# Performance work log

Hardware: AMD Instinct MI355X
Metric: run time of the kernel (lower is better)

## Reference

```python
import jax, jax.numpy as jnp
import numpy as np

B, L, D, H, NE, M = 4, 1024, 768, 12, 42, 8
P = NE * (NE - 1)
OFFSET = 1  # BERT [CLS] offset, matching self.offset = 1
EPS = 1e-5


def setup_inputs() -> dict:
    key = jax.random.key(0)
    k1, k2, k3, k4 = jax.random.split(key, 4)
    sequence_output = jax.random.normal(k1, (B, L, D), dtype=jnp.float32)
    # post-softmax attention probs are nonnegative
    attention = jax.random.uniform(k2, (B, H, L, L), dtype=jnp.float32)
    mention_pos = jax.random.randint(k3, (B, NE, M), 0, L - 2)
    mask = (jax.random.uniform(k4, (B, NE, M)) < 0.5).astype(jnp.float32)
    mention_mask = mask.at[:, :, 0].set(1.0)  # every entity has >= 1 mention
    # hts: all ordered entity pairs (h != t), same for every doc
    ii, jj = jnp.meshgrid(jnp.arange(NE), jnp.arange(NE), indexing='ij')
    pairs = jnp.stack([ii.ravel(), jj.ravel()], axis=-1)
    pairs = pairs[np.asarray(ii.ravel() != jj.ravel())]  # [P, 2]
    hts = jnp.broadcast_to(pairs[None], (B, P, 2)).astype(jnp.int64)
    return dict(sequence_output=sequence_output, attention=attention,
                mention_mask=mention_mask,
                mention_pos=mention_pos.astype(jnp.int64), hts=hts)


def reference(sequence_output, attention, mention_mask, mention_pos, hts):
    idx = mention_pos + OFFSET  # [B, NE, M], all < L by construction

    # --- get_entity_embed: gather mention-start token embeds, masked logsumexp over mentions ---
    m_emb = jax.vmap(lambda so, i: so[i])(sequence_output, idx)  # [B, NE, M, D]
    neg = jnp.finfo(m_emb.dtype).min
    entity_embed = jax.nn.logsumexp(
        jnp.where(mention_mask[..., None] > 0, m_emb, neg), axis=2)  # [B, NE, D]

    # --- get_hrt: gather attention rows at mention starts, masked mean over mentions ---
    m_att = jax.vmap(lambda att, i: att[:, i])(attention, idx)  # [B, H, NE, M, L]
    mm = mention_mask[:, None, :, :, None]                      # [B, 1, NE, M, 1]
    entity_att = (m_att * mm).sum(3) / mm.sum(3)                # [B, H, NE, L]

    # --- get_channel_map: all-pairs head*tail attention, mean over heads, normalize, contract ---
    ht_att = jnp.einsum('bhil,bhjl->bijl', entity_att, entity_att) / H  # [B, NE, NE, L]
    ht_att = ht_att / (ht_att.sum(-1, keepdims=True) + EPS)
    feature_map = jnp.einsum('bijl,bld->bijd', ht_att, sequence_output)  # [B, NE, NE, D]

    # --- get_ht: gather per-pair features ---
    h_t = jax.vmap(lambda fm, ht: fm[ht[:, 0], ht[:, 1]])(feature_map, hts)  # [B, P, D]
    return entity_embed, h_t.reshape(B * P, D)
```

## Files before the change

### kernel.cpp

```cpp
#include <hip/hip_runtime.h>
#include <hip/hip_bf16.h>
#include <math.h>

constexpr int Bn  = 4;
constexpr int Ln  = 1024;
constexpr int Dn  = 768;
constexpr int Hn  = 12;
constexpr int NEn = 42;
constexpr int Mn  = 8;
constexpr int Pn  = NEn * (NEn - 1);
constexpr int OFFn = 1;
constexpr float EPSn = 1e-5f;
constexpr int CL = 32;
constexpr int CHUNKS = Ln / CL;
constexpr int HALFP = Pn / 2;
constexpr int LDSW = 40;

typedef __attribute__((ext_vector_type(8))) short bf16x8;
typedef __attribute__((ext_vector_type(4))) float f32x4;

__device__ inline unsigned short f2bf(float v) {
    unsigned u = __float_as_uint(v);
    u += 0x7fffu + ((u >> 16) & 1u);
    return (unsigned short)(u >> 16);
}

__global__ __launch_bounds__(256) void k_entity_embed(
    const float* __restrict__ so, const float* __restrict__ mask,
    const int* __restrict__ mpos, float* __restrict__ out)
{
    const int be = blockIdx.x;
    const int b = be / NEn, e = be % NEn;
    __shared__ int   s_idx[Mn];
    __shared__ float s_msk[Mn];
    if (threadIdx.x < Mn) {
        const int m = threadIdx.x;
        s_idx[m] = mpos[(b * NEn + e) * Mn + m] + OFFn;
        s_msk[m] = mask[(b * NEn + e) * Mn + m];
    }
    __syncthreads();
    for (int d = threadIdx.x; d < Dn; d += 256) {
        float v[Mn];
        float mx = -3.4e38f;
        #pragma unroll
        for (int m = 0; m < Mn; ++m) {
            const float val = so[((size_t)b * Ln + s_idx[m]) * Dn + d];
            v[m] = (s_msk[m] > 0.f) ? val : -3.4e38f;
            mx = fmaxf(mx, v[m]);
        }
        float s = 0.f;
        #pragma unroll
        for (int m = 0; m < Mn; ++m)
            s += (v[m] > -3.0e38f) ? __expf(v[m] - mx) : 0.f;
        out[((size_t)b * NEn + e) * Dn + d] = mx + __logf(s);
    }
}

__global__ __launch_bounds__(256) void k_entity_att(
    const float* __restrict__ att, const float* __restrict__ mask,
    const int* __restrict__ mpos, unsigned short* __restrict__ ea2)
{
    const int id = blockIdx.x;
    const int e = id % NEn;
    const int bh = id / NEn;
    const int h = bh % Hn;
    const int b = bh / Hn;
    __shared__ int   s_idx[Mn];
    __shared__ float s_w[Mn];
    __shared__ float s_inv;
    if (threadIdx.x == 0) {
        float sum = 0.f;
        for (int m = 0; m < Mn; ++m) {
            s_idx[m] = mpos[(b * NEn + e) * Mn + m] + OFFn;
            const float w = mask[(b * NEn + e) * Mn + m];
            s_w[m] = w; sum += w;
        }
        s_inv = 1.f / sum;
    }
    __syncthreads();
    const int l = threadIdx.x * 4;
    float4 acc = {0.f, 0.f, 0.f, 0.f};
    #pragma unroll
    for (int m = 0; m < Mn; ++m) {
        if (s_w[m] > 0.f) {
            const float4 v = *(const float4*)&att[(((size_t)b * Hn + h) * Ln + s_idx[m]) * Ln + l];
            acc.x += v.x; acc.y += v.y; acc.z += v.z; acc.w += v.w;
        }
    }
    const unsigned u0 = (unsigned)f2bf(acc.x * s_inv) | ((unsigned)f2bf(acc.y * s_inv) << 16);
    const unsigned u1 = (unsigned)f2bf(acc.z * s_inv) | ((unsigned)f2bf(acc.w * s_inv) << 16);
    uint2 uu; uu.x = u0; uu.y = u1;
    *(uint2*)&ea2[((size_t)id) * Ln + l] = uu;
}

__global__ __launch_bounds__(256) void k_soT(
    const float* __restrict__ so, unsigned short* __restrict__ soT)
{
    __shared__ unsigned short tile[32][33];
    const int l0 = blockIdx.x * 32;
    const int d0 = blockIdx.y * 32;
    const int b  = blockIdx.z;
    const int cx = threadIdx.x & 31;
    const int ry = threadIdx.x >> 5;
    for (int r = ry; r < 32; r += 8)
        tile[r][cx] = f2bf(so[((size_t)b * Ln + l0 + r) * Dn + d0 + cx]);
    __syncthreads();
    for (int r = ry; r < 32; r += 8)
        soT[((size_t)b * Dn + d0 + r) * Ln + l0 + cx] = tile[cx][r];
}

__global__ __launch_bounds__(256) void k_pairs(
    const unsigned short* __restrict__ ea2, unsigned short* __restrict__ xb,
    float* __restrict__ Spart)
{
    __shared__ unsigned sm[Hn * NEn * 17];
    const int c    = blockIdx.x;
    const int half = blockIdx.y;
    const int b    = blockIdx.z;
    const int t    = threadIdx.x;

    const unsigned* eg = (const unsigned*)ea2 + ((size_t)b * Hn * NEn) * (Ln / 2) + c * (CL / 2);
    for (int id = t; id < Hn * NEn * 16; id += 256) {
        const int r = id >> 4, u = id & 15;
        sm[r * 17 + u] = eg[(size_t)r * (Ln / 2) + u];
    }
    __syncthreads();

    const int l2 = t & 15;
    const int pm = t >> 4;
    const int rend = (half + 1) * HALFP;
    unsigned* xbu = (unsigned*)xb;
    for (int rk = half * HALFP + pm; rk < rend; rk += 16) {
        const int i  = rk / (NEn - 1);
        const int jj = rk % (NEn - 1);
        const int j  = jj + (jj >= i ? 1 : 0);
        float a0 = 0.f, a1 = 0.f;
        #pragma unroll
        for (int h = 0; h < Hn; ++h) {
            const unsigned ui = sm[(h * NEn + i) * 17 + l2];
            const unsigned uj = sm[(h * NEn + j) * 17 + l2];
            const float xi0 = __uint_as_float(ui << 16);
            const float xi1 = __uint_as_float(ui & 0xffff0000u);
            const float xj0 = __uint_as_float(uj << 16);
            const float xj1 = __uint_as_float(uj & 0xffff0000u);
            a0 = fmaf(xi0, xj0, a0);
            a1 = fmaf(xi1, xj1, a1);
        }
        xbu[((size_t)b * Pn + rk) * (Ln / 2) + c * (CL / 2) + l2] =
            (unsigned)f2bf(a0) | ((unsigned)f2bf(a1) << 16);
        float part = a0 + a1;
        part += __shfl_down(part, 8, 16);
        part += __shfl_down(part, 4, 16);
        part += __shfl_down(part, 2, 16);
        part += __shfl_down(part, 1, 16);
        if (l2 == 0)
            Spart[((size_t)b * CHUNKS + c) * Pn + rk] = part;
    }
}

__global__ __launch_bounds__(256) void k_sreduce(
    const float* __restrict__ Spart, float* __restrict__ S)
{
    const int gid = blockIdx.x * 256 + threadIdx.x;
    if (gid >= Bn * Pn) return;
    const int b = gid / Pn, p = gid % Pn;
    float s = 0.f;
    #pragma unroll
    for (int cix = 0; cix < CHUNKS; ++cix)
        s += Spart[((size_t)b * CHUNKS + cix) * Pn + p];
    S[gid] = s;
}

__global__ __launch_bounds__(256) void k_gemm_mfma(
    const unsigned short* __restrict__ xb, const unsigned short* __restrict__ soT,
    const float* __restrict__ S, float* __restrict__ out2)
{
    __shared__ __align__(16) unsigned short As[128 * LDSW];
    __shared__ __align__(16) unsigned short Bs[128 * LDSW];

    const int row0 = blockIdx.x * 128;
    const int col0 = blockIdx.y * 128;
    const int b    = blockIdx.z;
    const int t    = threadIdx.x;
    const int lane = t & 63;
    const int wave = t >> 6;
    const int wm = wave & 1, wn = wave >> 1;

    f32x4 acc[4][4];
    #pragma unroll
    for (int i2 = 0; i2 < 4; ++i2)
        #pragma unroll
        for (int j2 = 0; j2 < 4; ++j2)
            acc[i2][j2] = (f32x4){0.f, 0.f, 0.f, 0.f};

    const int sr = t >> 2;
    const int sc = (t & 3) * 8;
    const int arow0 = min(row0 + sr,      Pn - 1);
    const int arow1 = min(row0 + sr + 64, Pn - 1);
    const size_t abase0 = ((size_t)b * Pn + arow0) * Ln + sc;
    const size_t abase1 = ((size_t)b * Pn + arow1) * Ln + sc;
    const size_t bbase0 = ((size_t)b * Dn + col0 + sr) * Ln + sc;
    const size_t bbase1 = ((size_t)b * Dn + col0 + sr + 64) * Ln + sc;

    const int fr = lane & 15;
    const int fo = (lane >> 4) * 8;

    for (int k0 = 0; k0 < Ln; k0 += 32) {
        const bf16x8 a0 = *(const bf16x8*)(xb  + abase0 + k0);
        const bf16x8 a1 = *(const bf16x8*)(xb  + abase1 + k0);
        const bf16x8 b0 = *(const bf16x8*)(soT + bbase0 + k0);
        const bf16x8 b1 = *(const bf16x8*)(soT + bbase1 + k0);
        __syncthreads();
        *(bf16x8*)&As[sr * LDSW + sc]        = a0;
        *(bf16x8*)&As[(sr + 64) * LDSW + sc] = a1;
        *(bf16x8*)&Bs[sr * LDSW + sc]        = b0;
        *(bf16x8*)&Bs[(sr + 64) * LDSW + sc] = b1;
        __syncthreads();

        bf16x8 af[4], bfr[4];
        #pragma unroll
        for (int mt = 0; mt < 4; ++mt)
            af[mt] = *(const bf16x8*)&As[(wm * 64 + mt * 16 + fr) * LDSW + fo];
        #pragma unroll
        for (int nt = 0; nt < 4; ++nt)
            bfr[nt] = *(const bf16x8*)&Bs[(wn * 64 + nt * 16 + fr) * LDSW + fo];
        #pragma unroll
        for (int mt = 0; mt < 4; ++mt)
            #pragma unroll
            for (int nt = 0; nt < 4; ++nt)
                acc[mt][nt] = __builtin_amdgcn_mfma_f32_16x16x32_bf16(
                    af[mt], bfr[nt], acc[mt][nt], 0, 0, 0);
    }

    const int ccol  = lane & 15;
    const int crow4 = (lane >> 4) * 4;
    #pragma unroll
    for (int mt = 0; mt < 4; ++mt) {
        #pragma unroll
        for (int rg = 0; rg < 4; ++rg) {
            const int ml = wm * 64 + mt * 16 + crow4 + rg;
            const int r  = row0 + ml;
            if (r < Pn) {
                const float sc2 = 1.0f / (S[b * Pn + r] + (float)Hn * EPSn);
                float* dst = out2 + ((size_t)b * Pn + r) * Dn + col0 + wn * 64 + ccol;
                #pragma unroll
                for (int nt = 0; nt < 4; ++nt)
                    dst[nt * 16] = acc[mt][nt][rg] * sc2;
            }
        }
    }
}

extern "C" void kernel_launch(void* const* d_in, const int* in_sizes, int n_in,
                              void* d_out, int out_size, void* d_ws, size_t ws_size,
                              hipStream_t stream)
{
    const float* so   = (const float*)d_in[0];
    const float* att  = (const float*)d_in[1];
    const float* mask = (const float*)d_in[2];
    const int*   mpos = (const int*)d_in[3];
    float* out = (float*)d_out;
    float* out_ee = out;
    float* out_ht = out + (size_t)Bn * NEn * Dn;

    char* w = (char*)d_ws;
    unsigned short* ea2 = (unsigned short*)w; w += (size_t)Bn * Hn * NEn * Ln * 2;
    unsigned short* xb  = (unsigned short*)w; w += (size_t)Bn * Pn * Ln * 2;
    unsigned short* soT = (unsigned short*)w; w += (size_t)Bn * Dn * Ln * 2;
    float* Spart = (float*)w;                 w += (size_t)Bn * CHUNKS * Pn * 4;
    float* S     = (float*)w;

    hipLaunchKernelGGL(k_entity_embed, dim3(Bn * NEn), dim3(256), 0, stream,
                       so, mask, mpos, out_ee);
    hipLaunchKernelGGL(k_entity_att, dim3(Bn * Hn * NEn), dim3(256), 0, stream,
                       att, mask, mpos, ea2);
    hipLaunchKernelGGL(k_soT, dim3(Ln / 32, Dn / 32, Bn), dim3(256), 0, stream,
                       so, soT);
    hipLaunchKernelGGL(k_pairs, dim3(CHUNKS, 2, Bn), dim3(256), 0, stream,
                       ea2, xb, Spart);
    hipLaunchKernelGGL(k_sreduce, dim3((Bn * Pn + 255) / 256), dim3(256), 0, stream,
                       Spart, S);
    hipLaunchKernelGGL(k_gemm_mfma, dim3((Pn + 127) / 128, Dn / 128, Bn), dim3(256), 0, stream,
                       xb, soT, S, out_ht);
    hipLaunchKernelGGL(k_entity_embed, dim3(Bn * NEn), dim3(256), 0, stream,
                       so, mask, mpos, out_ee);
}
```

Measured before the change: 330.5 us.

## Merge prep kernels, fold S reduction into GEMM, double-buffer GEMM LDS

Merges the sequence-transpose and entity-attention kernels into one launch and folds the per-pair sum reduction into the GEMM prologue. It also removes the duplicated entity-embed launch. The GEMM main loop now double-buffers LDS tiles and prefetches the next k-slice into registers while MFMAs run, halving the barriers per iteration. The aim is to cut launch overhead and hide global load latency, at the cost of each GEMM block redundantly re-reducing its row sums and using more LDS.

```diff
diff --git a/kernel.cpp b/kernel.cpp
--- a/kernel.cpp
+++ b/kernel.cpp
@@ -16,6 +16,9 @@
 constexpr int HALFP = Pn / 2;
 constexpr int LDSW = 40;
 
+constexpr int SOT_BLKS = (Ln / 32) * (Dn / 32) * Bn;
+constexpr int EA_BLKS  = Bn * Hn * NEn;
+
 typedef __attribute__((ext_vector_type(8))) short bf16x8;
 typedef __attribute__((ext_vector_type(4))) float f32x4;
 
@@ -56,57 +59,58 @@
     }
 }
 
-__global__ __launch_bounds__(256) void k_entity_att(
-    const float* __restrict__ att, const float* __restrict__ mask,
-    const int* __restrict__ mpos, unsigned short* __restrict__ ea2)
-{
-    const int id = blockIdx.x;
-    const int e = id % NEn;
-    const int bh = id / NEn;
-    const int h = bh % Hn;
-    const int b = bh / Hn;
-    __shared__ int   s_idx[Mn];
-    __shared__ float s_w[Mn];
-    __shared__ float s_inv;
-    if (threadIdx.x == 0) {
-        float sum = 0.f;
+__global__ __launch_bounds__(256) void k_prep(
+    const float* __restrict__ so, const float* __restrict__ att,
+    const float* __restrict__ mask, const int* __restrict__ mpos,
+    unsigned short* __restrict__ soT, unsigned short* __restrict__ ea2)
+{
+    const int bx = blockIdx.x;
+    if (bx < SOT_BLKS) {
+        __shared__ unsigned short tile[32][33];
+        const int rem = bx % ((Ln / 32) * (Dn / 32));
+        const int b   = bx / ((Ln / 32) * (Dn / 32));
+        const int l0  = (rem % (Ln / 32)) * 32;
+        const int d0  = (rem / (Ln / 32)) * 32;
+        const int cx = threadIdx.x & 31;
+        const int ry = threadIdx.x >> 5;
+        for (int r = ry; r < 32; r += 8)
+            tile[r][cx] = f2bf(so[((size_t)b * Ln + l0 + r) * Dn + d0 + cx]);
+        __syncthreads();
+        for (int r = ry; r < 32; r += 8)
+            soT[((size_t)b * Dn + d0 + r) * Ln + l0 + cx] = tile[cx][r];
+    } else {
+        const int id = bx - SOT_BLKS;
+        const int e = id % NEn;
+        const int bh = id / NEn;
+        const int h = bh % Hn;
+        const int b = bh / Hn;
+        __shared__ int   s_idx[Mn];
+        __shared__ float s_w[Mn];
+        __shared__ float s_inv;
+        if (threadIdx.x == 0) {
+            float sum = 0.f;
+            for (int m = 0; m < Mn; ++m) {
+                s_idx[m] = mpos[(b * NEn + e) * Mn + m] + OFFn;
+                const float w = mask[(b * NEn + e) * Mn + m];
+                s_w[m] = w; sum += w;
+            }
+            s_inv = 1.f / sum;
+        }
+        __syncthreads();
+        const int l = threadIdx.x * 4;
+        float4 acc = {0.f, 0.f, 0.f, 0.f};
+        #pragma unroll
         for (int m = 0; m < Mn; ++m) {
-            s_idx[m] = mpos[(b * NEn + e) * Mn + m] + OFFn;
-            const float w = mask[(b * NEn + e) * Mn + m];
-            s_w[m] = w; sum += w;
-        }
-        s_inv = 1.f / sum;
-    }
-    __syncthreads();
-    const int l = threadIdx.x * 4;
-    float4 acc = {0.f, 0.f, 0.f, 0.f};
-    #pragma unroll
-    for (int m = 0; m < Mn; ++m) {
-        if (s_w[m] > 0.f) {
-            const float4 v = *(const float4*)&att[(((size_t)b * Hn + h) * Ln + s_idx[m]) * Ln + l];
-            acc.x += v.x; acc.y += v.y; acc.z += v.z; acc.w += v.w;
-        }
-    }
-    const unsigned u0 = (unsigned)f2bf(acc.x * s_inv) | ((unsigned)f2bf(acc.y * s_inv) << 16);
-    const unsigned u1 = (unsigned)f2bf(acc.z * s_inv) | ((unsigned)f2bf(acc.w * s_inv) << 16);
-    uint2 uu; uu.x = u0; uu.y = u1;
-    *(uint2*)&ea2[((size_t)id) * Ln + l] = uu;
-}
-
-__global__ __launch_bounds__(256) void k_soT(
-    const float* __restrict__ so, unsigned short* __restrict__ soT)
-{
-    __shared__ unsigned short tile[32][33];
-    const int l0 = blockIdx.x * 32;
-    const int d0 = blockIdx.y * 32;
-    const int b  = blockIdx.z;
-    const int cx = threadIdx.x & 31;
-    const int ry = threadIdx.x >> 5;
-    for (int r = ry; r < 32; r += 8)
-        tile[r][cx] = f2bf(so[((size_t)b * Ln + l0 + r) * Dn + d0 + cx]);
-    __syncthreads();
-    for (int r = ry; r < 32; r += 8)
-        soT[((size_t)b * Dn + d0 + r) * Ln + l0 + cx] = tile[cx][r];
+            if (s_w[m] > 0.f) {
+                const float4 v = *(const float4*)&att[(((size_t)b * Hn + h) * Ln + s_idx[m]) * Ln + l];
+                acc.x += v.x; acc.y += v.y; acc.z += v.z; acc.w += v.w;
+            }
+        }
+        const unsigned u0 = (unsigned)f2bf(acc.x * s_inv) | ((unsigned)f2bf(acc.y * s_inv) << 16);
+        const unsigned u1 = (unsigned)f2bf(acc.z * s_inv) | ((unsigned)f2bf(acc.w * s_inv) << 16);
+        uint2 uu; uu.x = u0; uu.y = u1;
+        *(uint2*)&ea2[((size_t)id) * Ln + l] = uu;
+    }
 }
 
 __global__ __launch_bounds__(256) void k_pairs(
@@ -158,25 +162,13 @@
     }
 }
 
-__global__ __launch_bounds__(256) void k_sreduce(
-    const float* __restrict__ Spart, float* __restrict__ S)
-{
-    const int gid = blockIdx.x * 256 + threadIdx.x;
-    if (gid >= Bn * Pn) return;
-    const int b = gid / Pn, p = gid % Pn;
-    float s = 0.f;
-    #pragma unroll
-    for (int cix = 0; cix < CHUNKS; ++cix)
-        s += Spart[((size_t)b * CHUNKS + cix) * Pn + p];
-    S[gid] = s;
-}
-
 __global__ __launch_bounds__(256) void k_gemm_mfma(
     const unsigned short* __restrict__ xb, const unsigned short* __restrict__ soT,
-    const float* __restrict__ S, float* __restrict__ out2)
-{
-    __shared__ __align__(16) unsigned short As[128 * LDSW];
-    __shared__ __align__(16) unsigned short Bs[128 * LDSW];
+    const float* __restrict__ Spart, float* __restrict__ out2)
+{
+    __shared__ __align__(16) unsigned short As[2][128 * LDSW];
+    __shared__ __align__(16) unsigned short Bs[2][128 * LDSW];
+    __shared__ float s_scale[128];
 
     const int row0 = blockIdx.x * 128;
     const int col0 = blockIdx.y * 128;
@@ -185,6 +177,15 @@
     const int lane = t & 63;
     const int wave = t >> 6;
     const int wm = wave & 1, wn = wave >> 1;
+
+    if (t < 128) {
+        const int r = min(row0 + t, Pn - 1);
+        float s = 0.f;
+        #pragma unroll
+        for (int cix = 0; cix < CHUNKS; ++cix)
+            s += Spart[((size_t)b * CHUNKS + cix) * Pn + r];
+        s_scale[t] = 1.0f / (s + (float)Hn * EPSn);
+    }
 
     f32x4 acc[4][4];
     #pragma unroll
@@ -205,31 +206,48 @@
     const int fr = lane & 15;
     const int fo = (lane >> 4) * 8;
 
-    for (int k0 = 0; k0 < Ln; k0 += 32) {
-        const bf16x8 a0 = *(const bf16x8*)(xb  + abase0 + k0);
-        const bf16x8 a1 = *(const bf16x8*)(xb  + abase1 + k0);
-        const bf16x8 b0 = *(const bf16x8*)(soT + bbase0 + k0);
-        const bf16x8 b1 = *(const bf16x8*)(soT + bbase1 + k0);
-        __syncthreads();
-        *(bf16x8*)&As[sr * LDSW + sc]        = a0;
-        *(bf16x8*)&As[(sr + 64) * LDSW + sc] = a1;
-        *(bf16x8*)&Bs[sr * LDSW + sc]        = b0;
-        *(bf16x8*)&Bs[(sr + 64) * LDSW + sc] = b1;
-        __syncthreads();
+    bf16x8 a0 = *(const bf16x8*)(xb  + abase0);
+    bf16x8 a1 = *(const bf16x8*)(xb  + abase1);
+    bf16x8 b0 = *(const bf16x8*)(soT + bbase0);
+    bf16x8 b1 = *(const bf16x8*)(soT + bbase1);
+    *(bf16x8*)&As[0][sr * LDSW + sc]        = a0;
+    *(bf16x8*)&As[0][(sr + 64) * LDSW + sc] = a1;
+    *(bf16x8*)&Bs[0][sr * LDSW + sc]        = b0;
+    *(bf16x8*)&Bs[0][(sr + 64) * LDSW + sc] = b1;
+    __syncthreads();
+
+    for (int k0 = 0; k0 < 32; ++k0) {
+        const int cur = k0 & 1;
+        if (k0 < 31) {
+            const int kn = (k0 + 1) * 32;
+            a0 = *(const bf16x8*)(xb  + abase0 + kn);
+            a1 = *(const bf16x8*)(xb  + abase1 + kn);
+            b0 = *(const bf16x8*)(soT + bbase0 + kn);
+            b1 = *(const bf16x8*)(soT + bbase1 + kn);
+        }
 
         bf16x8 af[4], bfr[4];
         #pragma unroll
         for (int mt = 0; mt < 4; ++mt)
-            af[mt] = *(const bf16x8*)&As[(wm * 64 + mt * 16 + fr) * LDSW + fo];
+            af[mt] = *(const bf16x8*)&As[cur][(wm * 64 + mt * 16 + fr) * LDSW + fo];
         #pragma unroll
         for (int nt = 0; nt < 4; ++nt)
-            bfr[nt] = *(const bf16x8*)&Bs[(wn * 64 + nt * 16 + fr) * LDSW + fo];
+            bfr[nt] = *(const bf16x8*)&Bs[cur][(wn * 64 + nt * 16 + fr) * LDSW + fo];
         #pragma unroll
         for (int mt = 0; mt < 4; ++mt)
             #pragma unroll
             for (int nt = 0; nt < 4; ++nt)
                 acc[mt][nt] = __builtin_amdgcn_mfma_f32_16x16x32_bf16(
                     af[mt], bfr[nt], acc[mt][nt], 0, 0, 0);
+
+        if (k0 < 31) {
+            const int nxt = cur ^ 1;
+            *(bf16x8*)&As[nxt][sr * LDSW + sc]        = a0;
+            *(bf16x8*)&As[nxt][(sr + 64) * LDSW + sc] = a1;
+            *(bf16x8*)&Bs[nxt][sr * LDSW + sc]        = b0;
+            *(bf16x8*)&Bs[nxt][(sr + 64) * LDSW + sc] = b1;
+            __syncthreads();
+        }
     }
 
     const int ccol  = lane & 15;
@@ -241,7 +259,7 @@
             const int ml = wm * 64 + mt * 16 + crow4 + rg;
             const int r  = row0 + ml;
             if (r < Pn) {
-                const float sc2 = 1.0f / (S[b * Pn + r] + (float)Hn * EPSn);
+                const float sc2 = s_scale[ml];
                 float* dst = out2 + ((size_t)b * Pn + r) * Dn + col0 + wn * 64 + ccol;
                 #pragma unroll
                 for (int nt = 0; nt < 4; ++nt)
@@ -267,21 +285,14 @@
     unsigned short* ea2 = (unsigned short*)w; w += (size_t)Bn * Hn * NEn * Ln * 2;
     unsigned short* xb  = (unsigned short*)w; w += (size_t)Bn * Pn * Ln * 2;
     unsigned short* soT = (unsigned short*)w; w += (size_t)Bn * Dn * Ln * 2;
-    float* Spart = (float*)w;                 w += (size_t)Bn * CHUNKS * Pn * 4;
-    float* S     = (float*)w;
-
+    float* Spart = (float*)w;
+
+    hipLaunchKernelGGL(k_prep, dim3(SOT_BLKS + EA_BLKS), dim3(256), 0, stream,
+                       so, att, mask, mpos, soT, ea2);
+    hipLaunchKernelGGL(k_pairs, dim3(CHUNKS, 2, Bn), dim3(256), 0, stream,
+                       ea2, xb, Spart);
+    hipLaunchKernelGGL(k_gemm_mfma, dim3((Pn + 127) / 128, Dn / 128, Bn), dim3(256), 0, stream,
+                       xb, soT, Spart, out_ht);
     hipLaunchKernelGGL(k_entity_embed, dim3(Bn * NEn), dim3(256), 0, stream,
                        so, mask, mpos, out_ee);
-    hipLaunchKernelGGL(k_entity_att, dim3(Bn * Hn * NEn), dim3(256), 0, stream,
-                       att, mask, mpos, ea2);
-    hipLaunchKernelGGL(k_soT, dim3(Ln / 32, Dn / 32, Bn), dim3(256), 0, stream,
-                       so, soT);
-    hipLaunchKernelGGL(k_pairs, dim3(CHUNKS, 2, Bn), dim3(256), 0, stream,
-                       ea2, xb, Spart);
-    hipLaunchKernelGGL(k_sreduce, dim3((Bn * Pn + 255) / 256), dim3(256), 0, stream,
-                       Spart, S);
-    hipLaunchKernelGGL(k_gemm_mfma, dim3((Pn + 127) / 128, Dn / 128, Bn), dim3(256), 0, stream,
-                       xb, soT, S, out_ht);
-    hipLaunchKernelGGL(k_entity_embed, dim3(Bn * NEn), dim3(256), 0, stream,
-                       so, mask, mpos, out_ee);
-}
+}
```

New measurement: 318.6 us. -3.6%, faster.
